# Kernel optimization log

Hardware: AMD Instinct MI355X
Metric: run time of the kernel (lower is better)

The kernel has to match this reference:

```python
import jax, jax.numpy as jnp
import numpy as np

N_NODES = 100000
N_EDGES = 1600000
N_FEAT = 128
HIDDEN = 128
EMB = 256
N_GROUPS = 16
N_GRAPHS = 512


def gcn_conv(x, edge_index, W, b, num_nodes):
    # PyG GCNConv: x' = D^{-1/2} (A + I) D^{-1/2} (x W) + b
    h = x @ W                                   # [N, out]
    loop = jnp.arange(num_nodes, dtype=edge_index.dtype)
    src = jnp.concatenate([edge_index[0], loop])
    dst = jnp.concatenate([edge_index[1], loop])
    ones = jnp.ones(src.shape[0], dtype=h.dtype)
    deg = jax.ops.segment_sum(ones, dst, num_segments=num_nodes)  # >=1 due to self loops
    dinv = jax.lax.rsqrt(deg)
    norm = dinv[src] * dinv[dst]                # [E+N]
    msg = h[src] * norm[:, None]                # gather + scale
    out = jax.ops.segment_sum(msg, dst, num_segments=num_nodes)   # scatter-add
    return out + b


def global_mean_pool(x, batch, num_graphs):
    s = jax.ops.segment_sum(x, batch, num_segments=num_graphs)
    cnt = jax.ops.segment_sum(jnp.ones(x.shape[0], dtype=x.dtype), batch, num_segments=num_graphs)
    return s / jnp.maximum(cnt, 1.0)[:, None]


def setup_inputs() -> dict:
    key = jax.random.key(0)
    ks = jax.random.split(key, 10)
    x = jax.random.normal(ks[0], (N_NODES, N_FEAT), dtype=jnp.float32)
    edge_index = jax.random.randint(ks[1], (2, N_EDGES), 0, N_NODES, dtype=jnp.int64 if jax.config.jax_enable_x64 else jnp.int32)
    batch = jnp.sort(jax.random.randint(ks[2], (N_NODES,), 0, N_GRAPHS))
    def glorot(k, shape):
        lim = np.sqrt(6.0 / (shape[0] + shape[1]))
        return jax.random.uniform(k, shape, jnp.float32, -lim, lim)
    W1 = glorot(ks[3], (N_FEAT, HIDDEN)); b1 = jnp.zeros((HIDDEN,), jnp.float32)
    W2 = glorot(ks[4], (HIDDEN, EMB));    b2 = jnp.zeros((EMB,), jnp.float32)
    Wg = glorot(ks[5], (EMB, N_GROUPS));  bg = jnp.zeros((N_GROUPS,), jnp.float32)
    return {"x": x, "edge_index": edge_index, "batch": batch, "num_graphs": N_GRAPHS,
            "W1": W1, "b1": b1, "W2": W2, "b2": b2, "Wg": Wg, "bg": bg}


def reference(x, edge_index, batch, num_graphs, W1, b1, W2, b2, Wg, bg):
    n = x.shape[0]
    h = jax.nn.relu(gcn_conv(x, edge_index, W1, b1, n))
    # dropout(p=0.5) is identity in eval mode
    h = gcn_conv(h, edge_index, W2, b2, n)
    emb = global_mean_pool(h, batch, num_graphs)      # [G, EMB]
    group_logits = emb @ Wg + bg                      # [G, N_GROUPS]
    return (emb, group_logits)
```

## Files before the change

### kernel.cpp

```cpp
#include <hip/hip_runtime.h>
#include <hip/hip_fp16.h>


#define TPB 256
#define CHUNK 4096
#define MAXB 512

typedef _Float16 half8 __attribute__((ext_vector_type(8)));
typedef float floatx4 __attribute__((ext_vector_type(4)));

__device__ __forceinline__ void exscan512(int* a, int* part, int t) {
    int x0 = a[2 * t], x1 = a[2 * t + 1];
    part[t] = x0 + x1;
    __syncthreads();
    for (int off = 1; off < 256; off <<= 1) {
        int v = (t >= off) ? part[t - off] : 0;
        __syncthreads();
        part[t] += v;
        __syncthreads();
    }
    int base = (t > 0) ? part[t - 1] : 0;
    a[2 * t] = base;
    a[2 * t + 1] = base + x0;
    __syncthreads();
}

__global__ __launch_bounds__(256) void k1_bucket(const int* __restrict__ ei, int E,
                                                 int B, int nchunks,
                                                 uint2* __restrict__ sorted,
                                                 int* __restrict__ histT,
                                                 int* __restrict__ sstartT,
                                                 int* __restrict__ bucketTot) {
    __shared__ int hcnt[MAXB], hoff[MAXB], hcur[MAXB], part[256];
    int c = blockIdx.x, t = threadIdx.x;
    int e0 = c * CHUNK;
    int m = E - e0; if (m > CHUNK) m = CHUNK;
    for (int i = t; i < MAXB; i += 256) { hcnt[i] = 0; hcur[i] = 0; }
    __syncthreads();
    for (int i = t; i < m; i += 256)
        atomicAdd(&hcnt[ei[E + e0 + i] >> 8], 1);
    __syncthreads();
    for (int i = t; i < MAXB; i += 256) hoff[i] = hcnt[i];
    __syncthreads();
    exscan512(hoff, part, t);
    for (int i = t; i < B; i += 256) {
        histT[(size_t)i * nchunks + c]   = hcnt[i];
        sstartT[(size_t)i * nchunks + c] = e0 + hoff[i];
        if (hcnt[i] > 0) atomicAdd(&bucketTot[i], hcnt[i]);
    }
    __syncthreads();
    for (int i = t; i < m; i += 256) {
        int src = ei[e0 + i], dst = ei[E + e0 + i];
        int b = dst >> 8;
        int pos = e0 + hoff[b] + atomicAdd(&hcur[b], 1);
        sorted[pos] = make_uint2((unsigned)src, (unsigned)dst);
    }
}

__global__ void k2_scanB(const int* __restrict__ bucketTot, int B,
                         int* __restrict__ bucketBase) {
    __shared__ int a[MAXB], part[256];
    int t = threadIdx.x;
    a[t]       = (t < B) ? bucketTot[t] : 0;
    a[t + 256] = (t + 256 < B) ? bucketTot[t + 256] : 0;
    __syncthreads();
    exscan512(a, part, t);
    if (t < B) bucketBase[t] = a[t];
    if (t + 256 < B) bucketBase[t + 256] = a[t + 256];
    if (t == 255) bucketBase[B] = part[255];
}

__global__ __launch_bounds__(256) void k3_scatter(const uint2* __restrict__ sorted,
                                                  const int* __restrict__ histT,
                                                  const int* __restrict__ sstartT,
                                                  const int* __restrict__ bucketBase,
                                                  const int* __restrict__ batch,
                                                  int* __restrict__ adj,
                                                  int* __restrict__ offs,
                                                  int* __restrict__ deg,
                                                  float* __restrict__ dinv,
                                                  int* __restrict__ cnt,
                                                  int n, int nchunks) {
    __shared__ int sliceS[MAXB], sliceOff[MAXB], part[256];
    __shared__ int ncnt[256], noff[512], ncur[256];
    int b = blockIdx.x, t = threadIdx.x;
    int vb = b << 8;
    for (int i = t; i < MAXB; i += 256) {
        sliceOff[i] = (i < nchunks) ? histT[(size_t)b * nchunks + i] : 0;
        sliceS[i]   = (i < nchunks) ? sstartT[(size_t)b * nchunks + i] : 0;
    }
    ncnt[t] = 0;
    __syncthreads();
    exscan512(sliceOff, part, t);
    int T = part[255];
    for (int i = t; i < T; i += 256) {
        int lo = 0, hi = nchunks - 1;
        while (lo < hi) {
            int mid = (lo + hi + 1) >> 1;
            if (sliceOff[mid] <= i) lo = mid; else hi = mid - 1;
        }
        uint2 e = sorted[sliceS[lo] + (i - sliceOff[lo])];
        atomicAdd(&ncnt[(int)e.y - vb], 1);
    }
    __syncthreads();
    for (int i = t; i < 512; i += 256) noff[i] = (i < 256) ? ncnt[i] : 0;
    __syncthreads();
    exscan512(noff, part, t);
    int base = bucketBase[b];
    int v = vb + t;
    if (v < n) {
        int dg = ncnt[t];
        offs[v] = base + noff[t];
        deg[v]  = dg;
        dinv[v] = rsqrtf((float)(dg + 1));
        atomicAdd(&cnt[batch[v]], 1);
    }
    ncur[t] = 0;
    __syncthreads();
    for (int i = t; i < T; i += 256) {
        int lo = 0, hi = nchunks - 1;
        while (lo < hi) {
            int mid = (lo + hi + 1) >> 1;
            if (sliceOff[mid] <= i) lo = mid; else hi = mid - 1;
        }
        uint2 e = sorted[sliceS[lo] + (i - sliceOff[lo])];
        int r = (int)e.y - vb;
        int pos = base + noff[r] + atomicAdd(&ncur[r], 1);
        adj[pos] = (int)e.x;
    }
}

__global__ void prep_wt(const float* __restrict__ W, __half* __restrict__ Wt) {
    int t = blockIdx.x * blockDim.x + threadIdx.x;
    int c = t & 127, k = t >> 7;
    Wt[c * 128 + k] = __float2half(W[(size_t)k * 128 + c]);
}

__global__ __launch_bounds__(256) void gemm1_mfma(const float* __restrict__ X,
                                                  const __half* __restrict__ Wt,
                                                  const float* __restrict__ dinv,
                                                  __half* __restrict__ out, int n) {
    __shared__ __align__(16) unsigned char As[64 * 128 * 2];
    __shared__ __align__(16) unsigned char Bs[128 * 128 * 2];
    int t = threadIdx.x;
    int wid = t >> 6, lane = t & 63;
    int qw = lane >> 4, lr = lane & 15;
    int rowBase = blockIdx.x * 64;

#pragma unroll
    for (int c = 0; c < 4; ++c) {
        int id = c * 256 + t;
        int r = id >> 4, kc = id & 15;
        int gr = rowBase + r;
        float4 x0, x1;
        if (gr < n) {
            const float4* src = (const float4*)(X + (size_t)gr * 128 + kc * 8);
            x0 = src[0]; x1 = src[1];
        } else {
            x0 = make_float4(0.f, 0.f, 0.f, 0.f); x1 = x0;
        }
        __half2 h0 = __floats2half2_rn(x0.x, x0.y);
        __half2 h1 = __floats2half2_rn(x0.z, x0.w);
        __half2 h2 = __floats2half2_rn(x1.x, x1.y);
        __half2 h3 = __floats2half2_rn(x1.z, x1.w);
        uint4 w;
        w.x = *(unsigned int*)&h0; w.y = *(unsigned int*)&h1;
        w.z = *(unsigned int*)&h2; w.w = *(unsigned int*)&h3;
        int byte = (r * 256 + kc * 16) ^ ((r & 7) << 4);
        *(uint4*)(As + byte) = w;
    }
#pragma unroll
    for (int c = 0; c < 8; ++c) {
        int id = c * 256 + t;
        int cr = id >> 4, kc = id & 15;
        uint4 w = *(const uint4*)(Wt + (size_t)cr * 128 + kc * 8);
        int byte = (cr * 256 + kc * 16) ^ ((cr & 7) << 4);
        *(uint4*)(Bs + byte) = w;
    }
    __syncthreads();

    floatx4 acc[4][2] = {};
#pragma unroll
    for (int ks = 0; ks < 4; ++ks) {
        int kb = ks * 32 + qw * 8;
        half8 a[4], b[2];
#pragma unroll
        for (int m = 0; m < 4; ++m) {
            int row = m * 16 + lr;
            int byte = (row * 256 + kb * 2) ^ ((row & 7) << 4);
            a[m] = *(const half8*)(As + byte);
        }
#pragma unroll
        for (int nn = 0; nn < 2; ++nn) {
            int col = wid * 32 + nn * 16 + lr;
            int byte = (col * 256 + kb * 2) ^ ((col & 7) << 4);
            b[nn] = *(const half8*)(Bs + byte);
        }
#pragma unroll
        for (int m = 0; m < 4; ++m)
#pragma unroll
            for (int nn = 0; nn < 2; ++nn)
                acc[m][nn] = __builtin_amdgcn_mfma_f32_16x16x32_f16(a[m], b[nn], acc[m][nn], 0, 0, 0);
    }

#pragma unroll
    for (int m = 0; m < 4; ++m) {
#pragma unroll
        for (int q = 0; q < 4; ++q) {
            int gr = rowBase + m * 16 + qw * 4 + q;
            if (gr < n) {
                float dv = dinv[gr];
#pragma unroll
                for (int nn = 0; nn < 2; ++nn) {
                    int col = wid * 32 + nn * 16 + lr;
                    out[(size_t)gr * 128 + col] = __float2half(acc[m][nn][q] * dv);
                }
            }
        }
    }
}

__device__ __forceinline__ void acc_h2(unsigned int rv, float2& a) {
    float2 f = __half22float2(*(__half2*)&rv);
    a.x += f.x; a.y += f.y;
}
#define ROWP(buf, u) ((const unsigned int*)((buf) + (size_t)(u) * 128))

#define PIPE_GATHER(buf)                                                        \
    int nb = d >> 3;                                                            \
    int i = nb << 3;                                                            \
    if (nb > 0) {                                                               \
        int u0 = adj[start+0], u1 = adj[start+1], u2 = adj[start+2],            \
            u3 = adj[start+3], u4 = adj[start+4], u5 = adj[start+5],            \
            u6 = adj[start+6], u7 = adj[start+7];                               \
        unsigned c0 = ROWP(buf,u0)[lane], c1 = ROWP(buf,u1)[lane];              \
        unsigned c2 = ROWP(buf,u2)[lane], c3 = ROWP(buf,u3)[lane];              \
        unsigned c4 = ROWP(buf,u4)[lane], c5 = ROWP(buf,u5)[lane];              \
        unsigned c6 = ROWP(buf,u6)[lane], c7 = ROWP(buf,u7)[lane];              \
        for (int b = 1; b < nb; ++b) {                                          \
            int bs = start + (b << 3);                                          \
            int t0 = adj[bs+0], t1 = adj[bs+1], t2 = adj[bs+2], t3 = adj[bs+3]; \
            int t4 = adj[bs+4], t5 = adj[bs+5], t6 = adj[bs+6], t7 = adj[bs+7]; \
            unsigned n0 = ROWP(buf,t0)[lane], n1 = ROWP(buf,t1)[lane];          \
            unsigned n2 = ROWP(buf,t2)[lane], n3 = ROWP(buf,t3)[lane];          \
            unsigned n4 = ROWP(buf,t4)[lane], n5 = ROWP(buf,t5)[lane];          \
            unsigned n6 = ROWP(buf,t6)[lane], n7 = ROWP(buf,t7)[lane];          \
            acc_h2(c0, a0); acc_h2(c1, a1); acc_h2(c2, a2); acc_h2(c3, a3);     \
            acc_h2(c4, a0); acc_h2(c5, a1); acc_h2(c6, a2); acc_h2(c7, a3);     \
            c0 = n0; c1 = n1; c2 = n2; c3 = n3;                                 \
            c4 = n4; c5 = n5; c6 = n6; c7 = n7;                                 \
        }                                                                       \
        acc_h2(c0, a0); acc_h2(c1, a1); acc_h2(c2, a2); acc_h2(c3, a3);         \
        acc_h2(c4, a0); acc_h2(c5, a1); acc_h2(c6, a2); acc_h2(c7, a3);         \
    }                                                                           \
    for (; i + 3 < d; i += 4) {                                                 \
        int u0 = adj[start+i+0], u1 = adj[start+i+1];                           \
        int u2 = adj[start+i+2], u3 = adj[start+i+3];                           \
        unsigned r0 = ROWP(buf,u0)[lane], r1 = ROWP(buf,u1)[lane];              \
        unsigned r2 = ROWP(buf,u2)[lane], r3 = ROWP(buf,u3)[lane];              \
        acc_h2(r0, a0); acc_h2(r1, a1); acc_h2(r2, a2); acc_h2(r3, a3);         \
    }                                                                           \
    for (; i < d; ++i) acc_h2(ROWP(buf, adj[start + i])[lane], a0);

__global__ void gather1(const __half* __restrict__ hs, const int* __restrict__ adj,
                        const int* __restrict__ offs, const int* __restrict__ deg,
                        const float* __restrict__ dinv, const float* __restrict__ b1,
                        __half* __restrict__ gs, int n) {
    int wave = threadIdx.x >> 6;
    int lane = threadIdx.x & 63;
    int v = blockIdx.x * 4 + wave;
    if (v >= n) return;
    float2 a0 = make_float2(0.f, 0.f), a1 = a0, a2 = a0, a3 = a0;
    acc_h2(ROWP(hs, v)[lane], a0);
    int start = __builtin_amdgcn_readfirstlane(offs[v]);
    int d     = __builtin_amdgcn_readfirstlane(deg[v]);
    PIPE_GATHER(hs)
    float accx = (a0.x + a1.x) + (a2.x + a3.x);
    float accy = (a0.y + a1.y) + (a2.y + a3.y);
    float dv = dinv[v];
    float2 bb = ((const float2*)b1)[lane];
    float g0 = fmaxf(accx * dv + bb.x, 0.f) * dv;
    float g1 = fmaxf(accy * dv + bb.y, 0.f) * dv;
    __half2 h = __floats2half2_rn(g0, g1);
    ((unsigned int*)(gs + (size_t)v * 128))[lane] = *(unsigned int*)&h;
}

__global__ void gather2_pool(const __half* __restrict__ gs, const int* __restrict__ adj,
                             const int* __restrict__ offs, const int* __restrict__ deg,
                             const float* __restrict__ dinv, const int* __restrict__ batch,
                             float* __restrict__ poolsum, int n) {
    int wave = threadIdx.x >> 6;
    int lane = threadIdx.x & 63;
    int v = blockIdx.x * 4 + wave;
    if (v >= n) return;
    float2 a0 = make_float2(0.f, 0.f), a1 = a0, a2 = a0, a3 = a0;
    acc_h2(ROWP(gs, v)[lane], a0);
    int start = __builtin_amdgcn_readfirstlane(offs[v]);
    int d     = __builtin_amdgcn_readfirstlane(deg[v]);
    PIPE_GATHER(gs)
    float accx = (a0.x + a1.x) + (a2.x + a3.x);
    float accy = (a0.y + a1.y) + (a2.y + a3.y);
    float dv = dinv[v];
    float* p = poolsum + (size_t)batch[v] * 128;
    atomicAdd(&p[lane * 2 + 0], accx * dv);
    atomicAdd(&p[lane * 2 + 1], accy * dv);
}

__global__ void head(const float* __restrict__ poolsum, const int* __restrict__ cnt,
                     const float* __restrict__ W2, const float* __restrict__ b2,
                     const float* __restrict__ Wg, const float* __restrict__ bg,
                     float* __restrict__ out, int G) {
    __shared__ float pm[128];
    __shared__ float emb[256];
    int g = blockIdx.x, t = threadIdx.x;
    float inv = 1.f / fmaxf((float)cnt[g], 1.f);
    if (t < 128) pm[t] = poolsum[(size_t)g * 128 + t] * inv;
    __syncthreads();
    float acc = b2[t];
    for (int k = 0; k < 128; ++k) acc += pm[k] * W2[k * 256 + t];
    out[(size_t)g * 256 + t] = acc;
    emb[t] = acc;
    __syncthreads();
    if (t < 16) {
        float a = bg[t];
        for (int j = 0; j < 256; ++j) a += emb[j] * Wg[j * 16 + t];
        out[(size_t)G * 256 + g * 16 + t] = a;
    }
}

extern "C" void kernel_launch(void* const* d_in, const int* in_sizes, int n_in,
                              void* d_out, int out_size, void* d_ws, size_t ws_size,
                              hipStream_t stream) {
    const float* x     = (const float*)d_in[0];
    const int*   ei    = (const int*)d_in[1];
    const int*   batch = (const int*)d_in[2];
    const float* W1    = (const float*)d_in[4];
    const float* b1    = (const float*)d_in[5];
    const float* W2    = (const float*)d_in[6];
    const float* b2    = (const float*)d_in[7];
    const float* Wg    = (const float*)d_in[8];
    const float* bg    = (const float*)d_in[9];
    float* out = (float*)d_out;

    int n = in_sizes[0] / 128;
    int E = in_sizes[1] / 2;
    int G = out_size / (256 + 16);
    int B = (n + 255) >> 8;
    int nchunks = (E + CHUNK - 1) / CHUNK;

    char* ws = (char*)d_ws;
    auto alloc = [&](size_t bytes) {
        char* p = ws;
        ws += (bytes + 255) & ~(size_t)255;
        return p;
    };
    int*    deg       = (int*)alloc((size_t)n * 4);
    float*  dinv      = (float*)alloc((size_t)n * 4);
    int*    offs      = (int*)alloc((size_t)n * 4);
    int*    adj       = (int*)alloc((size_t)E * 4);
    uint2*  sorted    = (uint2*)alloc((size_t)E * 8);
    int*    histT     = (int*)alloc((size_t)B * nchunks * 4);
    int*    sstartT   = (int*)alloc((size_t)B * nchunks * 4);
    int*    bucketTot = (int*)alloc((size_t)(B + 1) * 4);
    int*    bucketBase= (int*)alloc((size_t)(B + 1) * 4);
    int*    cnt       = (int*)alloc((size_t)G * 4);
    float*  poolsum   = (float*)alloc((size_t)G * 128 * 4);
    __half* Wt        = (__half*)alloc(128 * 128 * 2);
    __half* hs1       = (__half*)alloc((size_t)n * 128 * 2);
    __half* gs1       = (__half*)alloc((size_t)n * 128 * 2);

    hipMemsetAsync(bucketTot, 0, (size_t)(B + 1) * 4, stream);
    hipMemsetAsync(cnt, 0, (size_t)G * 4, stream);
    hipMemsetAsync(poolsum, 0, (size_t)G * 128 * 4, stream);

    k1_bucket<<<nchunks, 256, 0, stream>>>(ei, E, B, nchunks, sorted, histT, sstartT, bucketTot);
    k2_scanB<<<1, 256, 0, stream>>>(bucketTot, B, bucketBase);
    k3_scatter<<<B, 256, 0, stream>>>(sorted, histT, sstartT, bucketBase, batch,
                                      adj, offs, deg, dinv, cnt, n, nchunks);

    prep_wt<<<64, TPB, 0, stream>>>(W1, Wt);
    gemm1_mfma<<<(n + 63) / 64, 256, 0, stream>>>(x, Wt, dinv, hs1, n);
    gather1<<<(n + 3) / 4, 256, 0, stream>>>(hs1, adj, offs, deg, dinv, b1, gs1, n);
    gather2_pool<<<(n + 3) / 4, 256, 0, stream>>>(gs1, adj, offs, deg, dinv, batch, poolsum, n);
    head<<<G, 256, 0, stream>>>(poolsum, cnt, W2, b2, Wg, bg, out, G);
}
```

Measured before the change: 362.2 us.

## Split CSR scatter into sub-sliced degree/offset/scatter kernels and pre-reduce pool atomics

```diff
diff --git a/kernel.cpp b/kernel.cpp
--- a/kernel.cpp
+++ b/kernel.cpp
@@ -5,6 +5,7 @@
 #define TPB 256
 #define CHUNK 4096
 #define MAXB 512
+#define SUBS 8
 
 typedef _Float16 half8 __attribute__((ext_vector_type(8)));
 typedef float floatx4 __attribute__((ext_vector_type(4)));
@@ -70,62 +71,83 @@
     if (t == 255) bucketBase[B] = part[255];
 }
 
-__global__ __launch_bounds__(256) void k3_scatter(const uint2* __restrict__ sorted,
-                                                  const int* __restrict__ histT,
-                                                  const int* __restrict__ sstartT,
-                                                  const int* __restrict__ bucketBase,
-                                                  const int* __restrict__ batch,
-                                                  int* __restrict__ adj,
-                                                  int* __restrict__ offs,
-                                                  int* __restrict__ deg,
-                                                  float* __restrict__ dinv,
-                                                  int* __restrict__ cnt,
-                                                  int n, int nchunks) {
-    __shared__ int sliceS[MAXB], sliceOff[MAXB], part[256];
-    __shared__ int ncnt[256], noff[512], ncur[256];
+#define SLICE_SETUP                                                             \
+    int b = blockIdx.x, sub = blockIdx.y, t = threadIdx.x;                      \
+    int cpg = (nchunks + SUBS - 1) / SUBS;                                      \
+    int c0 = sub * cpg;                                                         \
+    int c1 = c0 + cpg; if (c1 > nchunks) c1 = nchunks;                          \
+    int nc = c1 - c0; if (nc < 0) nc = 0;                                       \
+    if (t < nc) {                                                               \
+        slen[t]   = histT[(size_t)b * nchunks + c0 + t];                        \
+        sstart[t] = sstartT[(size_t)b * nchunks + c0 + t];                      \
+    }                                                                           \
+    __syncthreads();                                                            \
+    if (t == 0) {                                                               \
+        int run = 0;                                                            \
+        for (int i2 = 0; i2 < nc; ++i2) { soff[i2] = run; run += slen[i2]; }    \
+        soff[nc] = run;                                                         \
+    }                                                                           \
+    __syncthreads();                                                            \
+    int T = soff[nc];
+
+#define SLICE_EDGE(i)                                                           \
+    int lo = 0, hi = nc - 1;                                                    \
+    while (lo < hi) { int mid = (lo + hi + 1) >> 1;                             \
+                      if (soff[mid] <= (i)) lo = mid; else hi = mid - 1; }      \
+    uint2 e = sorted[sstart[lo] + ((i) - soff[lo])];
+
+__global__ __launch_bounds__(256) void k3a_deg(const uint2* __restrict__ sorted,
+                                               const int* __restrict__ histT,
+                                               const int* __restrict__ sstartT,
+                                               int* __restrict__ deg,
+                                               int n, int nchunks) {
+    __shared__ int slen[64], sstart[64], soff[65];
+    __shared__ int ncnt[256];
+    SLICE_SETUP
+    ncnt[t] = 0;
+    __syncthreads();
+    int vb = b << 8;
+    for (int i = t; i < T; i += 256) {
+        SLICE_EDGE(i)
+        atomicAdd(&ncnt[(int)e.y - vb], 1);
+    }
+    __syncthreads();
+    int v = vb + t;
+    if (v < n && ncnt[t] > 0) atomicAdd(&deg[v], ncnt[t]);
+}
+
+__global__ __launch_bounds__(256) void k3b_offs(const int* __restrict__ deg,
+                                                const int* __restrict__ bucketBase,
+                                                const int* __restrict__ batch,
+                                                int* __restrict__ offs,
+                                                float* __restrict__ dinv,
+                                                int* __restrict__ cnt, int n) {
+    __shared__ int a[512], part[256];
     int b = blockIdx.x, t = threadIdx.x;
-    int vb = b << 8;
-    for (int i = t; i < MAXB; i += 256) {
-        sliceOff[i] = (i < nchunks) ? histT[(size_t)b * nchunks + i] : 0;
-        sliceS[i]   = (i < nchunks) ? sstartT[(size_t)b * nchunks + i] : 0;
-    }
-    ncnt[t] = 0;
-    __syncthreads();
-    exscan512(sliceOff, part, t);
-    int T = part[255];
-    for (int i = t; i < T; i += 256) {
-        int lo = 0, hi = nchunks - 1;
-        while (lo < hi) {
-            int mid = (lo + hi + 1) >> 1;
-            if (sliceOff[mid] <= i) lo = mid; else hi = mid - 1;
-        }
-        uint2 e = sorted[sliceS[lo] + (i - sliceOff[lo])];
-        atomicAdd(&ncnt[(int)e.y - vb], 1);
-    }
-    __syncthreads();
-    for (int i = t; i < 512; i += 256) noff[i] = (i < 256) ? ncnt[i] : 0;
-    __syncthreads();
-    exscan512(noff, part, t);
-    int base = bucketBase[b];
-    int v = vb + t;
+    int v = (b << 8) + t;
+    int dg = (v < n) ? deg[v] : 0;
+    a[t] = dg; a[t + 256] = 0;
+    __syncthreads();
+    exscan512(a, part, t);
     if (v < n) {
-        int dg = ncnt[t];
-        offs[v] = base + noff[t];
-        deg[v]  = dg;
+        offs[v] = bucketBase[b] + a[t];
         dinv[v] = rsqrtf((float)(dg + 1));
         atomicAdd(&cnt[batch[v]], 1);
     }
-    ncur[t] = 0;
-    __syncthreads();
+}
+
+__global__ __launch_bounds__(256) void k3c_scatter(const uint2* __restrict__ sorted,
+                                                   const int* __restrict__ histT,
+                                                   const int* __restrict__ sstartT,
+                                                   const int* __restrict__ offs,
+                                                   int* __restrict__ cursor,
+                                                   int* __restrict__ adj, int nchunks) {
+    __shared__ int slen[64], sstart[64], soff[65];
+    SLICE_SETUP
     for (int i = t; i < T; i += 256) {
-        int lo = 0, hi = nchunks - 1;
-        while (lo < hi) {
-            int mid = (lo + hi + 1) >> 1;
-            if (sliceOff[mid] <= i) lo = mid; else hi = mid - 1;
-        }
-        uint2 e = sorted[sliceS[lo] + (i - sliceOff[lo])];
-        int r = (int)e.y - vb;
-        int pos = base + noff[r] + atomicAdd(&ncur[r], 1);
+        SLICE_EDGE(i)
+        int dst = (int)e.y;
+        int pos = offs[dst] + atomicAdd(&cursor[dst], 1);
         adj[pos] = (int)e.x;
     }
 }
@@ -237,8 +259,8 @@
         unsigned c2 = ROWP(buf,u2)[lane], c3 = ROWP(buf,u3)[lane];              \
         unsigned c4 = ROWP(buf,u4)[lane], c5 = ROWP(buf,u5)[lane];              \
         unsigned c6 = ROWP(buf,u6)[lane], c7 = ROWP(buf,u7)[lane];              \
-        for (int b = 1; b < nb; ++b) {                                          \
-            int bs = start + (b << 3);                                          \
+        for (int bq = 1; bq < nb; ++bq) {                                       \
+            int bs = start + (bq << 3);                                         \
             int t0 = adj[bs+0], t1 = adj[bs+1], t2 = adj[bs+2], t3 = adj[bs+3]; \
             int t4 = adj[bs+4], t5 = adj[bs+5], t6 = adj[bs+6], t7 = adj[bs+7]; \
             unsigned n0 = ROWP(buf,t0)[lane], n1 = ROWP(buf,t1)[lane];          \
@@ -289,21 +311,38 @@
                              const int* __restrict__ offs, const int* __restrict__ deg,
                              const float* __restrict__ dinv, const int* __restrict__ batch,
                              float* __restrict__ poolsum, int n) {
-    int wave = threadIdx.x >> 6;
-    int lane = threadIdx.x & 63;
+    __shared__ float poolacc[128];
+    int t = threadIdx.x;
+    int wave = t >> 6;
+    int lane = t & 63;
+    if (t < 128) poolacc[t] = 0.f;
+    int gref = batch[blockIdx.x * 4];
+    __syncthreads();
     int v = blockIdx.x * 4 + wave;
-    if (v >= n) return;
-    float2 a0 = make_float2(0.f, 0.f), a1 = a0, a2 = a0, a3 = a0;
-    acc_h2(ROWP(gs, v)[lane], a0);
-    int start = __builtin_amdgcn_readfirstlane(offs[v]);
-    int d     = __builtin_amdgcn_readfirstlane(deg[v]);
-    PIPE_GATHER(gs)
-    float accx = (a0.x + a1.x) + (a2.x + a3.x);
-    float accy = (a0.y + a1.y) + (a2.y + a3.y);
-    float dv = dinv[v];
-    float* p = poolsum + (size_t)batch[v] * 128;
-    atomicAdd(&p[lane * 2 + 0], accx * dv);
-    atomicAdd(&p[lane * 2 + 1], accy * dv);
+    if (v < n) {
+        float2 a0 = make_float2(0.f, 0.f), a1 = a0, a2 = a0, a3 = a0;
+        acc_h2(ROWP(gs, v)[lane], a0);
+        int start = __builtin_amdgcn_readfirstlane(offs[v]);
+        int d     = __builtin_amdgcn_readfirstlane(deg[v]);
+        PIPE_GATHER(gs)
+        float accx = (a0.x + a1.x) + (a2.x + a3.x);
+        float accy = (a0.y + a1.y) + (a2.y + a3.y);
+        float dv = dinv[v];
+        int g = batch[v];
+        if (g == gref) {
+            atomicAdd(&poolacc[lane * 2 + 0], accx * dv);
+            atomicAdd(&poolacc[lane * 2 + 1], accy * dv);
+        } else {
+            float* p = poolsum + (size_t)g * 128;
+            atomicAdd(&p[lane * 2 + 0], accx * dv);
+            atomicAdd(&p[lane * 2 + 1], accy * dv);
+        }
+    }
+    __syncthreads();
+    if (t < 128) {
+        float s = poolacc[t];
+        if (s != 0.f) atomicAdd(&poolsum[(size_t)gref * 128 + t], s);
+    }
 }
 
 __global__ void head(const float* __restrict__ poolsum, const int* __restrict__ cnt,
@@ -357,6 +396,7 @@
     int*    deg       = (int*)alloc((size_t)n * 4);
     float*  dinv      = (float*)alloc((size_t)n * 4);
     int*    offs      = (int*)alloc((size_t)n * 4);
+    int*    cursor    = (int*)alloc((size_t)n * 4);
     int*    adj       = (int*)alloc((size_t)E * 4);
     uint2*  sorted    = (uint2*)alloc((size_t)E * 8);
     int*    histT     = (int*)alloc((size_t)B * nchunks * 4);
@@ -369,14 +409,17 @@
     __half* hs1       = (__half*)alloc((size_t)n * 128 * 2);
     __half* gs1       = (__half*)alloc((size_t)n * 128 * 2);
 
+    hipMemsetAsync(deg, 0, (size_t)n * 4, stream);
+    hipMemsetAsync(cursor, 0, (size_t)n * 4, stream);
     hipMemsetAsync(bucketTot, 0, (size_t)(B + 1) * 4, stream);
     hipMemsetAsync(cnt, 0, (size_t)G * 4, stream);
     hipMemsetAsync(poolsum, 0, (size_t)G * 128 * 4, stream);
 
     k1_bucket<<<nchunks, 256, 0, stream>>>(ei, E, B, nchunks, sorted, histT, sstartT, bucketTot);
     k2_scanB<<<1, 256, 0, stream>>>(bucketTot, B, bucketBase);
-    k3_scatter<<<B, 256, 0, stream>>>(sorted, histT, sstartT, bucketBase, batch,
-                                      adj, offs, deg, dinv, cnt, n, nchunks);
+    k3a_deg<<<dim3(B, SUBS), 256, 0, stream>>>(sorted, histT, sstartT, deg, n, nchunks);
+    k3b_offs<<<B, 256, 0, stream>>>(deg, bucketBase, batch, offs, dinv, cnt, n);
+    k3c_scatter<<<dim3(B, SUBS), 256, 0, stream>>>(sorted, histT, sstartT, offs, cursor, adj, nchunks);
 
     prep_wt<<<64, TPB, 0, stream>>>(W1, Wt);
     gemm1_mfma<<<(n + 63) / 64, 256, 0, stream>>>(x, Wt, dinv, hs1, n);
```

Result: no change. 367.7 us (+1.5%).
